# Optimization experiments

Hardware: AMD Instinct MI355X
Metric: run time of the kernel (lower is better)

The kernel has to match this reference:

```python
import jax, jax.numpy as jnp
import numpy as np

EPS = 1.1920929e-07  # float32 eps, matches torch.finfo(torch.float32).eps
QMAX = 127.0         # 2**(8-1)-1 for 8-bit symmetric quantization
NUM_HEADS = 12


def _round_ste(x):
    return x + jax.lax.stop_gradient(jnp.round(x) - x)


def _floor_ste(x):
    return x + jax.lax.stop_gradient(jnp.floor(x) - x)


def _act_quant(x):
    # per-tensor symmetric 8-bit (QuantAct + SymmetricQuantFunction)
    s = jax.lax.stop_gradient(jnp.maximum(jnp.max(jnp.abs(x)) / QMAX, EPS))
    return jnp.clip(_round_ste(x / s), -QMAX - 1.0, QMAX), s


def _weight_quant(w):
    # per-output-channel symmetric 8-bit (scale.view(-1,1) path in linear_quantize)
    s = jax.lax.stop_gradient(jnp.maximum(jnp.max(jnp.abs(w), axis=1) / QMAX, EPS))
    return jnp.clip(_round_ste(w / s[:, None]), -QMAX - 1.0, QMAX), s


def _fixedpoint_requant(pre_act, pre_s, z_s):
    # fixedpoint_mul: requantize int accumulator (value pre_act on scale pre_s)
    # onto scale z_s using a 31-bit mantissa/exponent decomposition (batch_frexp).
    def int_path(pa):
        z_int = jnp.round(pa / pre_s)
        ns = pre_s / z_s
        e = jnp.floor(jnp.log2(ns)) + 1.0          # frexp exponent: ns = m * 2**e, m in [0.5,1)
        m = jnp.floor(ns * jnp.exp2(-e) * 2.0 ** 31 + 0.5)  # ROUND_HALF_UP mantissa * 2**31
        out = jnp.round(z_int * m * jnp.exp2(e - 31.0))
        return jnp.clip(out, -QMAX - 1.0, QMAX)
    hard = jax.lax.stop_gradient(int_path(pre_act))
    soft = pre_act / z_s                            # STE backward: grad / z_scaling_factor
    return soft + jax.lax.stop_gradient(hard - soft)


def _int_softmax(x_int, sf, output_bit=8, n=15):
    # IntSoftmax (shiftmax) with int_exp_shift; x_int = logits / sf (integer-valued)
    x_int = x_int - jnp.max(x_int, axis=-1, keepdims=True)
    x_int = x_int + _floor_ste(x_int / 2.0) - _floor_ste(x_int / 16.0)
    x0 = jax.lax.stop_gradient(jnp.floor(-1.0 / sf))
    x_int = jnp.maximum(x_int, n * x0)
    q = _floor_ste(x_int / x0)
    r = x_int - x0 * q
    exp_int = jnp.clip(_floor_ste((r / 2.0 - x0) * jnp.exp2(n - q)), 0.0, None)
    esum = jnp.minimum(jnp.sum(exp_int, axis=-1, keepdims=True), 2.0 ** 31 - 1.0)
    factor = _floor_ste((2.0 ** 31 - 1.0) / esum)
    exp_int = _floor_ste(exp_int * factor / 2.0 ** (31 - output_bit + 1))
    return exp_int, 1.0 / 2.0 ** (output_bit - 1)


def setup_inputs() -> dict:
    key = jax.random.key(0)
    k1, k2, k3, k4, k5 = jax.random.split(key, 5)
    B, N, C = 8, 577, 768
    return {
        "x": jax.random.normal(k1, (B, N, C), dtype=jnp.float32),
        "w_qkv": jax.random.normal(k2, (3 * C, C), dtype=jnp.float32) * 0.02,
        "b_qkv": jax.random.normal(k3, (3 * C,), dtype=jnp.float32) * 0.01,
        "w_proj": jax.random.normal(k4, (C, C), dtype=jnp.float32) * 0.02,
        "b_proj": jax.random.normal(k5, (C,), dtype=jnp.float32) * 0.01,
    }


def reference(x, w_qkv, b_qkv, w_proj, b_proj):
    B, N, C = x.shape
    H = NUM_HEADS
    D = C // H
    # ---- quantize input activation and qkv weight, integer GEMM ----
    x_int, s_x = _act_quant(x)                         # [B,N,C] int-valued, scalar scale
    wq_int, s_wq = _weight_quant(w_qkv)                # [3C,C], per-channel scale [3C]
    acc_s = s_x * s_wq                                 # accumulator scale [3C]
    qkv_int = jnp.einsum('bnc,oc->bno', x_int, wq_int) + _round_ste(b_qkv / acc_s)
    qkv_f = qkv_int * acc_s                            # dequantized qkv [B,N,3C]
    # ---- requantize qkv to per-tensor 8-bit via fixed-point mul ----
    s_qkv = jax.lax.stop_gradient(jnp.maximum(jnp.max(jnp.abs(qkv_f)) / QMAX, EPS))
    qkv8 = _fixedpoint_requant(qkv_f, acc_s, s_qkv)    # int8-valued [B,N,3C]
    qkv8 = qkv8.reshape(B, N, 3, H, D).transpose(2, 0, 3, 1, 4)
    q, k, v = qkv8[0], qkv8[1], qkv8[2]                # each [B,H,N,D]
    # ---- integer attention logits; float scale carries head_dim**-0.5 ----
    attn_int = jnp.einsum('bhnd,bhmd->bhnm', q, k)
    s_attn = s_qkv * s_qkv * (D ** -0.5)
    sm_int, s_sm = _int_softmax(attn_int, s_attn)      # int probs on scale 1/128
    # ---- integer attn @ v ----
    ctx_int = jnp.einsum('bhnm,bhmd->bhnd', sm_int, v)
    ctx_f = (ctx_int * (s_sm * s_qkv)).transpose(0, 2, 1, 3).reshape(B, N, C)
    s_ctx = jax.lax.stop_gradient(jnp.maximum(jnp.max(jnp.abs(ctx_f)) / QMAX, EPS))
    ctx8 = _fixedpoint_requant(ctx_f, s_sm * s_qkv, s_ctx)
    # ---- quantized output projection ----
    wp_int, s_wp = _weight_quant(w_proj)
    out_s = s_ctx * s_wp
    out_int = jnp.einsum('bnc,oc->bno', ctx8, wp_int) + _round_ste(b_proj / out_s)
    return out_int * out_s
```

## Files before the change

### kernel.cpp

```cpp
#include <hip/hip_runtime.h>
#include <math.h>

#define BQ 8
#define SEQ 577
#define CH 768
#define NH 12
#define HD 64
#define M_ROWS (BQ * SEQ)
#define QKV_CH (3 * CH)
#define NX (M_ROWS * CH)
#define EPSF 1.1920929e-07f
#define F2P31 2147483648.0f

#define VT_ROW 640
#define P_STRIDE 688

#define NSLOT 64
#define SLOT_STRIDE 16

typedef __attribute__((ext_vector_type(4))) int i32x4;

__device__ __forceinline__ float slot_scale(const unsigned* __restrict__ s) {
  float m = 0.f;
#pragma unroll
  for (int i = 0; i < NSLOT; ++i) m = fmaxf(m, __uint_as_float(s[i * SLOT_STRIDE]));
  return fmaxf(m / 127.0f, EPSF);
}

__device__ __forceinline__ void mfma_gemm_core_lds(
    const signed char* __restrict__ A, const signed char* __restrict__ Bm,
    signed char* As, signed char* Bs,
    int arow0, int bcol0, int w, int lane, i32x4 acc[4][4]) {
  int c = lane & 15, q = lane >> 4;
  int lr = lane >> 2;
  int ksb = (lane & 3) << 4;
  const signed char* Aw = As + ((w & 1) << 12);
  const signed char* Bw = Bs + ((w >> 1) << 12);
  for (int k0 = 0; k0 < CH; k0 += 64) {
#pragma unroll
    for (int u = 0; u < 2; ++u) {
      int row = (w << 5) + (u << 4) + lr;
      __builtin_amdgcn_global_load_lds(
          (const __attribute__((address_space(1))) void*)(A + (size_t)(arow0 + row) * CH + k0 + ksb),
          (__attribute__((address_space(3))) void*)(As + (w << 11) + (u << 10)),
          16, 0, 0);
      __builtin_amdgcn_global_load_lds(
          (const __attribute__((address_space(1))) void*)(Bm + (size_t)(bcol0 + row) * CH + k0 + ksb),
          (__attribute__((address_space(3))) void*)(Bs + (w << 11) + (u << 10)),
          16, 0, 0);
    }
    __syncthreads();
    i32x4 af[4], bf[4];
#pragma unroll
    for (int i = 0; i < 4; ++i)
      af[i] = *(const i32x4*)(Aw + (((i << 4) + c) << 6) + (q << 4));
#pragma unroll
    for (int j = 0; j < 4; ++j)
      bf[j] = *(const i32x4*)(Bw + (((j << 4) + c) << 6) + (q << 4));
#pragma unroll
    for (int i = 0; i < 4; ++i)
#pragma unroll
      for (int j = 0; j < 4; ++j)
        acc[i][j] = __builtin_amdgcn_mfma_i32_16x16x64_i8(af[i], bf[j], acc[i][j], 0, 0, 0);
    __syncthreads();
  }
}

__global__ __launch_bounds__(256) void k_prep(
    const float* __restrict__ x, const float* __restrict__ w_qkv,
    const float* __restrict__ w_proj,
    signed char* __restrict__ WQ8, float* __restrict__ SWQ,
    signed char* __restrict__ WP8, float* __restrict__ SWP,
    unsigned* __restrict__ mxx) {
  __shared__ float red[4];
  int blk = blockIdx.x, tid = threadIdx.x;
  if (blk < QKV_CH + CH) {
    const float* wr; signed char* w8; float* sw; int r;
    if (blk < QKV_CH) { r = blk; wr = w_qkv + (size_t)r * CH; w8 = WQ8 + (size_t)r * CH; sw = SWQ; }
    else { r = blk - QKV_CH; wr = w_proj + (size_t)r * CH; w8 = WP8 + (size_t)r * CH; sw = SWP; }
    const float4* wr4 = (const float4*)wr;
    float4 v = {0.f, 0.f, 0.f, 0.f};
    float m = 0.f;
    if (tid < CH / 4) {
      v = wr4[tid];
      m = fmaxf(fmaxf(fabsf(v.x), fabsf(v.y)), fmaxf(fabsf(v.z), fabsf(v.w)));
    }
#pragma unroll
    for (int o = 32; o; o >>= 1) m = fmaxf(m, __shfl_xor(m, o, 64));
    if ((tid & 63) == 0) red[tid >> 6] = m;
    __syncthreads();
    float mm = fmaxf(fmaxf(red[0], red[1]), fmaxf(red[2], red[3]));
    float s = fmaxf(mm / 127.0f, EPSF);
    if (tid == 0) sw[r] = s;
    if (tid < CH / 4) {
      int pk = 0;
#pragma unroll
      for (int u = 0; u < 4; ++u) {
        float xv = (u == 0) ? v.x : (u == 1) ? v.y : (u == 2) ? v.z : v.w;
        float q = rintf(xv / s);
        q = fminf(fmaxf(q, -128.f), 127.f);
        pk |= ((int)(signed char)q & 0xff) << (u * 8);
      }
      ((int*)w8)[tid] = pk;
    }
  } else {
    int ab = blk - (QKV_CH + CH);
    const float4* x4 = (const float4*)x;
    float m = 0.f;
    for (int i = ab * 256 + tid; i < NX / 4; i += 1024 * 256) {
      float4 v = x4[i];
      m = fmaxf(m, fmaxf(fmaxf(fabsf(v.x), fabsf(v.y)), fmaxf(fabsf(v.z), fabsf(v.w))));
    }
#pragma unroll
    for (int o = 32; o; o >>= 1) m = fmaxf(m, __shfl_xor(m, o, 64));
    if ((tid & 63) == 0) red[tid >> 6] = m;
    __syncthreads();
    if (tid == 0)
      atomicMax(&mxx[(ab & (NSLOT - 1)) * SLOT_STRIDE],
                __float_as_uint(fmaxf(fmaxf(red[0], red[1]), fmaxf(red[2], red[3]))));
  }
}

__global__ void k_aquant(const float* __restrict__ x, int n,
                         const unsigned* __restrict__ mxx, signed char* __restrict__ x8) {
  float s = slot_scale(mxx);
  int n4 = n >> 2;
  const float4* x4 = (const float4*)x;
  int* dst = (int*)x8;
  int stride = gridDim.x * blockDim.x;
  for (int i = blockIdx.x * blockDim.x + threadIdx.x; i < n4; i += stride) {
    float4 v = x4[i];
    int pk = 0;
#pragma unroll
    for (int u = 0; u < 4; ++u) {
      float xv = (u == 0) ? v.x : (u == 1) ? v.y : (u == 2) ? v.z : v.w;
      float q = rintf(xv / s);
      q = fminf(fmaxf(q, -128.f), 127.f);
      pk |= ((int)(signed char)q & 0xff) << (u * 8);
    }
    dst[i] = pk;
  }
}

__global__ __launch_bounds__(256) void k_gemm_qkv(
    const signed char* __restrict__ A, const signed char* __restrict__ Bm,
    const float* __restrict__ swq, const float* __restrict__ bias,
    const unsigned* __restrict__ mxx, int* __restrict__ Cq, unsigned* __restrict__ mxq) {
  __shared__ __align__(16) signed char As[8192], Bs[8192];
  __shared__ float red[4];
  int t = threadIdx.x;
  int lane = t & 63, w = t >> 6;
  int c = lane & 15, q = lane >> 4;
  int arow = blockIdx.y * 128 + (w & 1) * 64;
  int bcol = blockIdx.x * 128 + (w >> 1) * 64;
  i32x4 acc[4][4] = {};
  mfma_gemm_core_lds(A, Bm, As, Bs, blockIdx.y * 128, blockIdx.x * 128, w, lane, acc);
  float s_x = slot_scale(mxx);
  float lmax = 0.f;
#pragma unroll
  for (int j = 0; j < 4; ++j) {
    int ccol = bcol + j * 16 + c;
    float accs = s_x * swq[ccol];
    int bint = (int)rintf(bias[ccol] / accs);
#pragma unroll
    for (int i = 0; i < 4; ++i)
#pragma unroll
      for (int r = 0; r < 4; ++r) {
        int rr = arow + i * 16 + q * 4 + r;
        if (rr < M_ROWS) {
          int qv = acc[i][j][r] + bint;
          Cq[(size_t)rr * QKV_CH + ccol] = qv;
          lmax = fmaxf(lmax, fabsf((float)qv * accs));
        }
      }
  }
#pragma unroll
  for (int off = 32; off; off >>= 1) lmax = fmaxf(lmax, __shfl_xor(lmax, off, 64));
  if (lane == 0) red[w] = lmax;
  __syncthreads();
  if (t == 0)
    atomicMax(&mxq[((blockIdx.y * 18 + blockIdx.x) & (NSLOT - 1)) * SLOT_STRIDE],
              __float_as_uint(fmaxf(fmaxf(red[0], red[1]), fmaxf(red[2], red[3]))));
}

#define QK_BLKS 870
__global__ __launch_bounds__(256) void k_qkv_requant(
    const int* __restrict__ Cq, const float* __restrict__ swq,
    const unsigned* __restrict__ mxx, const unsigned* __restrict__ mxq,
    signed char* __restrict__ Q8, signed char* __restrict__ K8,
    signed char* __restrict__ VT8) {
  float s_x = slot_scale(mxx);
  float s_qkv = slot_scale(mxq);
  int blk = blockIdx.x, tid = threadIdx.x;
  if (blk < QK_BLKS) {
    int bx = blk % 6, by = blk / 6;
    int o = bx * 256 + tid;
    float accs = s_x * swq[o];
    float ns = accs / s_qkv;
    int e; float f = frexpf(ns, &e);
    float mm = floorf(f * F2P31 + 0.5f);
    float pw = __int_as_float((e + 96) << 23);
    int isK = (o >= CH);
    int rem = o - (isK ? CH : 0);
    int h = rem >> 6, d = rem & 63;
    signed char* dstb = isK ? K8 : Q8;
    int bn0 = by * 32;
    int bnend = min(bn0 + 32, M_ROWS);
    for (int bn = bn0; bn < bnend; ++bn) {
      int qv = Cq[(size_t)bn * QKV_CH + o];
      float qf = (float)qv * accs;
      float z = rintf(qf / accs);
      float t8 = rintf((z * mm) * pw);
      t8 = fminf(fmaxf(t8, -128.f), 127.f);
      int b = bn / SEQ, n = bn - b * SEQ;
      dstb[(((size_t)(b * NH + h) * SEQ + n) << 6) + d] = (signed char)t8;
    }
  } else {
    __shared__ __align__(16) signed char VTt[64 * 68];
    int vt = blk - QK_BLKS;
    int bh = vt / 10, n0 = (vt - bh * 10) * 64;
    int b = bh / NH, h = bh - b * NH;
    int od = tid & 63;
    int o = 2 * CH + h * 64 + od;
    float accs = s_x * swq[o];
    float ns = accs / s_qkv;
    int e; float f = frexpf(ns, &e);
    float mm = floorf(f * F2P31 + 0.5f);
    float pw = __int_as_float((e + 96) << 23);
    int nr = tid >> 6;
    for (int p = 0; p < 16; ++p) {
      int nl = nr * 16 + p;
      int n = n0 + nl;
      signed char v = 0;
      if (n < SEQ) {
        int qv = Cq[(size_t)(b * SEQ + n) * QKV_CH + o];
        float qf = (float)qv * accs;
        float z = rintf(qf / accs);
        float t8 = rintf((z * mm) * pw);
        t8 = fminf(fmaxf(t8, -128.f), 127.f);
        v = (signed char)t8;
      }
      VTt[od * 68 + nl] = v;
    }
    __syncthreads();
    int w16 = tid & 15, dr = tid >> 4;
#pragma unroll
    for (int pp = 0; pp < 4; ++pp) {
      int d = pp * 16 + dr;
      int val = *(const int*)&VTt[d * 68 + w16 * 4];
      *(int*)(VT8 + (size_t)bh * (64 * VT_ROW) + (size_t)d * VT_ROW + n0 + w16 * 4) = val;
    }
  }
}

__global__ __launch_bounds__(256, 4) void k_attn(
    const signed char* __restrict__ Q8, const signed char* __restrict__ K8,
    const signed char* __restrict__ VT8, const unsigned* __restrict__ mxq,
    int* __restrict__ ctxi, unsigned* __restrict__ mxc) {
  __shared__ __align__(16) unsigned char P[16 * P_STRIDE];
  __shared__ int Rmax[4][16];
  __shared__ unsigned long long Rsum[4][16];
  __shared__ float Rav[4];
  int tid = threadIdx.x;
  int t = tid & 63, wid = tid >> 6;
  int lin = blockIdx.x;
  int j = lin >> 3;
  int bh = (lin & 7) * 12 + j / 37;
  int qt = j % 37;
  int b = bh / NH, h = bh - b * NH;
  int col = t & 15, q4 = t >> 4;
  const signed char* Qb = Q8 + (((size_t)bh * SEQ + qt * 16 + col) << 6);
  i32x4 qa = *(const i32x4*)(Qb + q4 * 16);
  const signed char* Kb = K8 + ((size_t)bh * SEQ << 6);
  int kt0 = wid * 10;
  i32x4 sv[10];
  bool vld[10];
  int mx[4] = {-2147483647 - 1, -2147483647 - 1, -2147483647 - 1, -2147483647 - 1};
#pragma unroll
  for (int u = 0; u < 10; ++u) {
    int kt = kt0 + u;
    int krow = min(kt * 16 + col, SEQ - 1);
    const signed char* kr = Kb + ((size_t)krow << 6);
    i32x4 kb = *(const i32x4*)(kr + q4 * 16);
    i32x4 a = {0, 0, 0, 0};
    a = __builtin_amdgcn_mfma_i32_16x16x64_i8(qa, kb, a, 0, 0, 0);
    sv[u] = a;
    bool valid = (kt < 36) | ((kt == 36) & (col < 1));
    vld[u] = valid;
#pragma unroll
    for (int r = 0; r < 4; ++r)
      if (valid) mx[r] = max(mx[r], a[r]);
  }
#pragma unroll
  for (int r = 0; r < 4; ++r) {
    mx[r] = max(mx[r], __shfl_xor(mx[r], 1, 64));
    mx[r] = max(mx[r], __shfl_xor(mx[r], 2, 64));
    mx[r] = max(mx[r], __shfl_xor(mx[r], 4, 64));
    mx[r] = max(mx[r], __shfl_xor(mx[r], 8, 64));
  }
  if (col == 0) {
#pragma unroll
    for (int r = 0; r < 4; ++r) Rmax[wid][q4 * 4 + r] = mx[r];
  }
  __syncthreads();
#pragma unroll
  for (int r = 0; r < 4; ++r) {
    int row = q4 * 4 + r;
    mx[r] = max(max(Rmax[0][row], Rmax[1][row]), max(Rmax[2][row], Rmax[3][row]));
  }
  float s_qkv = slot_scale(mxq);
  float s_attn = (s_qkv * s_qkv) * 0.125f;
  float x0f = floorf(-1.0f / s_attn);
  int x0i = (int)x0f;
  int bi = -x0i;
  int nx0i = 15 * x0i;
  int twob = bi << 1;
  unsigned Mq = 0xFFFFFFFFu / (unsigned)bi + 1u;
  bool bOne = (Mq == 0u);
  unsigned long long su[4] = {0ull, 0ull, 0ull, 0ull};
#pragma unroll
  for (int u = 0; u < 10; ++u) {
#pragma unroll
    for (int r = 0; r < 4; ++r) {
      int d = sv[u][r] - mx[r];
      int xi = d + (d >> 1) - (d >> 4);
      xi = max(xi, nx0i);
      xi = min(xi, 0);
      unsigned a = (unsigned)(-xi);
      unsigned q = bOne ? a : __umulhi(a, Mq);
      int rr = (int)(a - q * (unsigned)bi);
      unsigned m = (unsigned)(twob - rr);
      unsigned ue = (m << 15) >> (q + 1);
      ue = vld[u] ? ue : 0u;
      su[r] += ue;
      sv[u][r] = (int)ue;
    }
  }
#pragma unroll
  for (int r = 0; r < 4; ++r) {
    su[r] += __shfl_xor(su[r], 1, 64);
    su[r] += __shfl_xor(su[r], 2, 64);
    su[r] += __shfl_xor(su[r], 4, 64);
    su[r] += __shfl_xor(su[r], 8, 64);
  }
  if (col == 0) {
#pragma unroll
    for (int r = 0; r < 4; ++r) Rsum[wid][q4 * 4 + r] = su[r];
  }
  __syncthreads();
  float fac[4];
#pragma unroll
  for (int r = 0; r < 4; ++r) {
    int row = q4 * 4 + r;
    unsigned long long dv = ((Rsum[0][row] + Rsum[1][row]) + Rsum[2][row]) + Rsum[3][row];
    float esum = fminf((float)dv, F2P31);
    fac[r] = floorf(F2P31 / esum);
  }
#pragma unroll
  for (int u = 0; u < 10; ++u) {
    int kt = kt0 + u;
#pragma unroll
    for (int r = 0; r < 4; ++r) {
      float e = (float)(unsigned)sv[u][r];
      int p = (int)floorf((e * fac[r]) * 5.9604644775390625e-08f);
      P[(q4 * 4 + r) * P_STRIDE + kt * 16 + col] = (unsigned char)p;
    }
  }
  __syncthreads();
  const signed char* Vb = VT8 + (size_t)bh * (64 * VT_ROW);
  i32x4 ac0 = {0, 0, 0, 0}, ac1 = {0, 0, 0, 0};
#pragma unroll
  for (int mc = 0; mc < 10; mc += 2) {
    i32x4 pa0 = *(const i32x4*)&P[col * P_STRIDE + mc * 64 + q4 * 16];
    i32x4 vb0 = *(const i32x4*)(Vb + (size_t)(wid * 16 + col) * VT_ROW + mc * 64 + q4 * 16);
    ac0 = __builtin_amdgcn_mfma_i32_16x16x64_i8(pa0, vb0, ac0, 0, 0, 0);
    i32x4 pa1 = *(const i32x4*)&P[col * P_STRIDE + (mc + 1) * 64 + q4 * 16];
    i32x4 vb1 = *(const i32x4*)(Vb + (size_t)(wid * 16 + col) * VT_ROW + (mc + 1) * 64 + q4 * 16);
    ac1 = __builtin_amdgcn_mfma_i32_16x16x64_i8(pa1, vb1, ac1, 0, 0, 0);
  }
  float pre_s = 0.0078125f * s_qkv;
  float avmax = 0.f;
#pragma unroll
  for (int r = 0; r < 4; ++r) {
    int n = qt * 16 + q4 * 4 + r;
    if (n < SEQ) {
      int cacc = ac0[r] + ac1[r];
      ctxi[((size_t)(b * SEQ + n)) * CH + h * 64 + wid * 16 + col] = cacc;
      avmax = fmaxf(avmax, fabsf((float)cacc * pre_s));
    }
  }
#pragma unroll
  for (int off = 32; off; off >>= 1) avmax = fmaxf(avmax, __shfl_xor(avmax, off, 64));
  if (t == 0) Rav[wid] = avmax;
  __syncthreads();
  if (tid == 0)
    atomicMax(&mxc[(blockIdx.x & (NSLOT - 1)) * SLOT_STRIDE],
              __float_as_uint(fmaxf(fmaxf(Rav[0], Rav[1]), fmaxf(Rav[2], Rav[3]))));
}

__global__ void k_ctx_requant(const int* __restrict__ ctxi, const unsigned* __restrict__ mxq,
                              const unsigned* __restrict__ mxc, signed char* __restrict__ C8) {
  float s_qkv = slot_scale(mxq);
  float pre_s = 0.0078125f * s_qkv;
  float s_ctx = slot_scale(mxc);
  float ns = pre_s / s_ctx;
  int e;
  float f = frexpf(ns, &e);
  float mm = floorf(f * F2P31 + 0.5f);
  float pw = exp2f((float)e - 31.0f);
  int total4 = (M_ROWS * CH) / 4;
  int stride = gridDim.x * blockDim.x;
  const int4* src = (const int4*)ctxi;
  int* dst = (int*)C8;
  for (int i = blockIdx.x * blockDim.x + threadIdx.x; i < total4; i += stride) {
    int4 v = src[i];
    int pk = 0;
#pragma unroll
    for (int u = 0; u < 4; ++u) {
      int cv = (u == 0) ? v.x : (u == 1) ? v.y : (u == 2) ? v.z : v.w;
      float cf = (float)cv * pre_s;
      float z = rintf(cf / pre_s);
      float t8 = rintf((z * mm) * pw);
      t8 = fminf(fmaxf(t8, -128.f), 127.f);
      pk |= ((int)(signed char)t8 & 0xff) << (u * 8);
    }
    dst[i] = pk;
  }
}

__global__ __launch_bounds__(256) void k_gemm_out(
    const signed char* __restrict__ A, const signed char* __restrict__ Bm,
    const float* __restrict__ swp, const float* __restrict__ bias,
    const unsigned* __restrict__ mxc, float* __restrict__ outp) {
  __shared__ __align__(16) signed char As[8192], Bs[8192];
  int t = threadIdx.x;
  int lane = t & 63, w = t >> 6;
  int c = lane & 15, q = lane >> 4;
  int arow = blockIdx.y * 128 + (w & 1) * 64;
  int bcol = blockIdx.x * 128 + (w >> 1) * 64;
  i32x4 acc[4][4] = {};
  mfma_gemm_core_lds(A, Bm, As, Bs, blockIdx.y * 128, blockIdx.x * 128, w, lane, acc);
  float s_ctx = slot_scale(mxc);
#pragma unroll
  for (int j = 0; j < 4; ++j) {
    int ccol = bcol + j * 16 + c;
    float outs = s_ctx * swp[ccol];
    int bint = (int)rintf(bias[ccol] / outs);
#pragma unroll
    for (int i = 0; i < 4; ++i)
#pragma unroll
      for (int r = 0; r < 4; ++r) {
        int rr = arow + i * 16 + q * 4 + r;
        if (rr < M_ROWS)
          outp[(size_t)rr * CH + ccol] = (float)(acc[i][j][r] + bint) * outs;
      }
  }
}

extern "C" void kernel_launch(void* const* d_in, const int* in_sizes, int n_in,
                              void* d_out, int out_size, void* d_ws, size_t ws_size,
                              hipStream_t stream) {
  const float* x = (const float*)d_in[0];
  const float* w_qkv = (const float*)d_in[1];
  const float* b_qkv = (const float*)d_in[2];
  const float* w_proj = (const float*)d_in[3];
  const float* b_proj = (const float*)d_in[4];
  float* outp = (float*)d_out;

  char* ws = (char*)d_ws;
  size_t off = 0;
  auto alloc = [&](size_t sz) -> char* {
    char* p = ws + off;
    off = (off + sz + 4095) & ~(size_t)4095;
    return p;
  };
  unsigned* mxx = (unsigned*)alloc(3 * NSLOT * SLOT_STRIDE * 4);
  unsigned* mxq = mxx + NSLOT * SLOT_STRIDE;
  unsigned* mxc = mxq + NSLOT * SLOT_STRIDE;
  float* SWQ = (float*)alloc(QKV_CH * 4);
  float* SWP = (float*)alloc(CH * 4);
  signed char* WQ8 = (signed char*)alloc((size_t)QKV_CH * CH);
  signed char* WP8 = (signed char*)alloc((size_t)CH * CH);
  signed char* X8  = (signed char*)alloc((size_t)(M_ROWS + 128) * CH);
  signed char* Q8  = (signed char*)alloc((size_t)M_ROWS * CH);
  signed char* K8  = (signed char*)alloc((size_t)M_ROWS * CH);
  signed char* VT8 = (signed char*)alloc((size_t)BQ * NH * 64 * VT_ROW);
  signed char* C8  = (signed char*)alloc((size_t)(M_ROWS + 128) * CH);
  int* QKVI = (int*)alloc((size_t)M_ROWS * QKV_CH * 4);
  int* CTXI = (int*)alloc((size_t)M_ROWS * CH * 4);
  (void)ws_size;

  hipMemsetAsync(mxx, 0, 3 * NSLOT * SLOT_STRIDE * 4, stream);
  k_prep<<<QKV_CH + CH + 1024, 256, 0, stream>>>(x, w_qkv, w_proj, WQ8, SWQ, WP8, SWP, mxx);
  k_aquant<<<2048, 256, 0, stream>>>(x, NX, mxx, X8);
  dim3 g1(QKV_CH / 128, (M_ROWS + 127) / 128);
  k_gemm_qkv<<<g1, 256, 0, stream>>>(X8, WQ8, SWQ, b_qkv, mxx, QKVI, mxq);
  k_qkv_requant<<<QK_BLKS + BQ * NH * 10, 256, 0, stream>>>(QKVI, SWQ, mxx, mxq, Q8, K8, VT8);
  k_attn<<<37 * BQ * NH, 256, 0, stream>>>(Q8, K8, VT8, mxq, CTXI, mxc);
  k_ctx_requant<<<1024, 256, 0, stream>>>(CTXI, mxq, mxc, C8);
  dim3 g2(CH / 128, (M_ROWS + 127) / 128);
  k_gemm_out<<<g2, 256, 0, stream>>>(C8, WP8, SWP, b_proj, mxc, outp);
}
```

Measured before the change: 198.9 us.

## Use single-wave 64x64 GEMM tiles and a global exp lookup table in attention

Both int8 GEMMs now run as one-wave blocks on 64x64 tiles instead of four-wave 128x128 tiles, which gives many more blocks but less operand reuse per block. Separately, the requant kernel gets extra blocks that build a global table of shift-exp values indexed by the clamped logit, and the attention softmax reads that table instead of computing a divide and shift per element. The table lookup trades arithmetic for scattered global/L2 reads, and the table is capped in size, which may not cover large scale ratios.

```diff
diff --git a/kernel.cpp b/kernel.cpp
--- a/kernel.cpp
+++ b/kernel.cpp
@@ -14,6 +14,7 @@
 
 #define VT_ROW 640
 #define P_STRIDE 688
+#define TBL_CAP 245761
 
 #define NSLOT 64
 #define SLOT_STRIDE 16
@@ -27,36 +28,34 @@
   return fmaxf(m / 127.0f, EPSF);
 }
 
-__device__ __forceinline__ void mfma_gemm_core_lds(
+__device__ __forceinline__ void mfma_gemm_core_w1(
     const signed char* __restrict__ A, const signed char* __restrict__ Bm,
     signed char* As, signed char* Bs,
-    int arow0, int bcol0, int w, int lane, i32x4 acc[4][4]) {
+    int arow0, int bcol0, int lane, i32x4 acc[4][4]) {
   int c = lane & 15, q = lane >> 4;
   int lr = lane >> 2;
   int ksb = (lane & 3) << 4;
-  const signed char* Aw = As + ((w & 1) << 12);
-  const signed char* Bw = Bs + ((w >> 1) << 12);
   for (int k0 = 0; k0 < CH; k0 += 64) {
 #pragma unroll
-    for (int u = 0; u < 2; ++u) {
-      int row = (w << 5) + (u << 4) + lr;
+    for (int u = 0; u < 4; ++u) {
+      int row = (u << 4) + lr;
       __builtin_amdgcn_global_load_lds(
           (const __attribute__((address_space(1))) void*)(A + (size_t)(arow0 + row) * CH + k0 + ksb),
-          (__attribute__((address_space(3))) void*)(As + (w << 11) + (u << 10)),
+          (__attribute__((address_space(3))) void*)(As + (u << 10)),
           16, 0, 0);
       __builtin_amdgcn_global_load_lds(
           (const __attribute__((address_space(1))) void*)(Bm + (size_t)(bcol0 + row) * CH + k0 + ksb),
-          (__attribute__((address_space(3))) void*)(Bs + (w << 11) + (u << 10)),
+          (__attribute__((address_space(3))) void*)(Bs + (u << 10)),
           16, 0, 0);
     }
     __syncthreads();
     i32x4 af[4], bf[4];
 #pragma unroll
     for (int i = 0; i < 4; ++i)
-      af[i] = *(const i32x4*)(Aw + (((i << 4) + c) << 6) + (q << 4));
+      af[i] = *(const i32x4*)(As + (((i << 4) + c) << 6) + (q << 4));
 #pragma unroll
     for (int j = 0; j < 4; ++j)
-      bf[j] = *(const i32x4*)(Bw + (((j << 4) + c) << 6) + (q << 4));
+      bf[j] = *(const i32x4*)(Bs + (((j << 4) + c) << 6) + (q << 4));
 #pragma unroll
     for (int i = 0; i < 4; ++i)
 #pragma unroll
@@ -142,19 +141,17 @@
   }
 }
 
-__global__ __launch_bounds__(256) void k_gemm_qkv(
+__global__ __launch_bounds__(64) void k_gemm_qkv(
     const signed char* __restrict__ A, const signed char* __restrict__ Bm,
     const float* __restrict__ swq, const float* __restrict__ bias,
     const unsigned* __restrict__ mxx, int* __restrict__ Cq, unsigned* __restrict__ mxq) {
-  __shared__ __align__(16) signed char As[8192], Bs[8192];
-  __shared__ float red[4];
-  int t = threadIdx.x;
-  int lane = t & 63, w = t >> 6;
+  __shared__ __align__(16) signed char As[4096], Bs[4096];
+  int lane = threadIdx.x;
   int c = lane & 15, q = lane >> 4;
-  int arow = blockIdx.y * 128 + (w & 1) * 64;
-  int bcol = blockIdx.x * 128 + (w >> 1) * 64;
+  int arow = blockIdx.y * 64;
+  int bcol = blockIdx.x * 64;
   i32x4 acc[4][4] = {};
-  mfma_gemm_core_lds(A, Bm, As, Bs, blockIdx.y * 128, blockIdx.x * 128, w, lane, acc);
+  mfma_gemm_core_w1(A, Bm, As, Bs, arow, bcol, lane, acc);
   float s_x = slot_scale(mxx);
   float lmax = 0.f;
 #pragma unroll
@@ -176,19 +173,18 @@
   }
 #pragma unroll
   for (int off = 32; off; off >>= 1) lmax = fmaxf(lmax, __shfl_xor(lmax, off, 64));
-  if (lane == 0) red[w] = lmax;
-  __syncthreads();
-  if (t == 0)
-    atomicMax(&mxq[((blockIdx.y * 18 + blockIdx.x) & (NSLOT - 1)) * SLOT_STRIDE],
-              __float_as_uint(fmaxf(fmaxf(red[0], red[1]), fmaxf(red[2], red[3]))));
+  if (lane == 0)
+    atomicMax(&mxq[((blockIdx.y * 36 + blockIdx.x) & (NSLOT - 1)) * SLOT_STRIDE],
+              __float_as_uint(lmax));
 }
 
 #define QK_BLKS 870
+#define V_BLKS (BQ * NH * 10)
 __global__ __launch_bounds__(256) void k_qkv_requant(
     const int* __restrict__ Cq, const float* __restrict__ swq,
     const unsigned* __restrict__ mxx, const unsigned* __restrict__ mxq,
     signed char* __restrict__ Q8, signed char* __restrict__ K8,
-    signed char* __restrict__ VT8) {
+    signed char* __restrict__ VT8, unsigned* __restrict__ TexpG) {
   float s_x = slot_scale(mxx);
   float s_qkv = slot_scale(mxq);
   int blk = blockIdx.x, tid = threadIdx.x;
@@ -215,7 +211,7 @@
       int b = bn / SEQ, n = bn - b * SEQ;
       dstb[(((size_t)(b * NH + h) * SEQ + n) << 6) + d] = (signed char)t8;
     }
-  } else {
+  } else if (blk < QK_BLKS + V_BLKS) {
     __shared__ __align__(16) signed char VTt[64 * 68];
     int vt = blk - QK_BLKS;
     int bh = vt / 10, n0 = (vt - bh * 10) * 64;
@@ -250,12 +246,26 @@
       int val = *(const int*)&VTt[d * 68 + w16 * 4];
       *(int*)(VT8 + (size_t)bh * (64 * VT_ROW) + (size_t)d * VT_ROW + n0 + w16 * 4) = val;
     }
+  } else {
+    int tb = blk - (QK_BLKS + V_BLKS);
+    float s_attn = (s_qkv * s_qkv) * 0.125f;
+    int bi = -(int)floorf(-1.0f / s_attn);
+    int tblN = min(15 * bi + 1, TBL_CAP);
+    unsigned Mq = 0xFFFFFFFFu / (unsigned)bi + 1u;
+    bool bOne = (Mq == 0u);
+    int twob = bi << 1;
+    for (int a = tb * 256 + tid; a < tblN; a += 4 * 256) {
+      unsigned q = bOne ? (unsigned)a : __umulhi((unsigned)a, Mq);
+      unsigned rr = (unsigned)a - q * (unsigned)bi;
+      TexpG[a] = ((unsigned)(twob - (int)rr) << 14) >> q;
+    }
   }
 }
 
 __global__ __launch_bounds__(256, 4) void k_attn(
     const signed char* __restrict__ Q8, const signed char* __restrict__ K8,
     const signed char* __restrict__ VT8, const unsigned* __restrict__ mxq,
+    const unsigned* __restrict__ TexpG,
     int* __restrict__ ctxi, unsigned* __restrict__ mxc) {
   __shared__ __align__(16) unsigned char P[16 * P_STRIDE];
   __shared__ int Rmax[4][16];
@@ -312,11 +322,7 @@
   float s_attn = (s_qkv * s_qkv) * 0.125f;
   float x0f = floorf(-1.0f / s_attn);
   int x0i = (int)x0f;
-  int bi = -x0i;
   int nx0i = 15 * x0i;
-  int twob = bi << 1;
-  unsigned Mq = 0xFFFFFFFFu / (unsigned)bi + 1u;
-  bool bOne = (Mq == 0u);
   unsigned long long su[4] = {0ull, 0ull, 0ull, 0ull};
 #pragma unroll
   for (int u = 0; u < 10; ++u) {
@@ -326,11 +332,7 @@
       int xi = d + (d >> 1) - (d >> 4);
       xi = max(xi, nx0i);
       xi = min(xi, 0);
-      unsigned a = (unsigned)(-xi);
-      unsigned q = bOne ? a : __umulhi(a, Mq);
-      int rr = (int)(a - q * (unsigned)bi);
-      unsigned m = (unsigned)(twob - rr);
-      unsigned ue = (m << 15) >> (q + 1);
+      unsigned ue = TexpG[-xi];
       ue = vld[u] ? ue : 0u;
       su[r] += ue;
       sv[u][r] = (int)ue;
@@ -428,18 +430,17 @@
   }
 }
 
-__global__ __launch_bounds__(256) void k_gemm_out(
+__global__ __launch_bounds__(64) void k_gemm_out(
     const signed char* __restrict__ A, const signed char* __restrict__ Bm,
     const float* __restrict__ swp, const float* __restrict__ bias,
     const unsigned* __restrict__ mxc, float* __restrict__ outp) {
-  __shared__ __align__(16) signed char As[8192], Bs[8192];
-  int t = threadIdx.x;
-  int lane = t & 63, w = t >> 6;
+  __shared__ __align__(16) signed char As[4096], Bs[4096];
+  int lane = threadIdx.x;
   int c = lane & 15, q = lane >> 4;
-  int arow = blockIdx.y * 128 + (w & 1) * 64;
-  int bcol = blockIdx.x * 128 + (w >> 1) * 64;
+  int arow = blockIdx.y * 64;
+  int bcol = blockIdx.x * 64;
   i32x4 acc[4][4] = {};
-  mfma_gemm_core_lds(A, Bm, As, Bs, blockIdx.y * 128, blockIdx.x * 128, w, lane, acc);
+  mfma_gemm_core_w1(A, Bm, As, Bs, arow, bcol, lane, acc);
   float s_ctx = slot_scale(mxc);
 #pragma unroll
   for (int j = 0; j < 4; ++j) {
@@ -477,6 +478,7 @@
   unsigned* mxx = (unsigned*)alloc(3 * NSLOT * SLOT_STRIDE * 4);
   unsigned* mxq = mxx + NSLOT * SLOT_STRIDE;
   unsigned* mxc = mxq + NSLOT * SLOT_STRIDE;
+  unsigned* TexpG = (unsigned*)alloc((size_t)TBL_CAP * 4);
   float* SWQ = (float*)alloc(QKV_CH * 4);
   float* SWP = (float*)alloc(CH * 4);
   signed char* WQ8 = (signed char*)alloc((size_t)QKV_CH * CH);
@@ -493,11 +495,11 @@
   hipMemsetAsync(mxx, 0, 3 * NSLOT * SLOT_STRIDE * 4, stream);
   k_prep<<<QKV_CH + CH + 1024, 256, 0, stream>>>(x, w_qkv, w_proj, WQ8, SWQ, WP8, SWP, mxx);
   k_aquant<<<2048, 256, 0, stream>>>(x, NX, mxx, X8);
-  dim3 g1(QKV_CH / 128, (M_ROWS + 127) / 128);
-  k_gemm_qkv<<<g1, 256, 0, stream>>>(X8, WQ8, SWQ, b_qkv, mxx, QKVI, mxq);
-  k_qkv_requant<<<QK_BLKS + BQ * NH * 10, 256, 0, stream>>>(QKVI, SWQ, mxx, mxq, Q8, K8, VT8);
-  k_attn<<<37 * BQ * NH, 256, 0, stream>>>(Q8, K8, VT8, mxq, CTXI, mxc);
+  dim3 g1(QKV_CH / 64, (M_ROWS + 63) / 64);
+  k_gemm_qkv<<<g1, 64, 0, stream>>>(X8, WQ8, SWQ, b_qkv, mxx, QKVI, mxq);
+  k_qkv_requant<<<QK_BLKS + V_BLKS + 4, 256, 0, stream>>>(QKVI, SWQ, mxx, mxq, Q8, K8, VT8, TexpG);
+  k_attn<<<37 * BQ * NH, 256, 0, stream>>>(Q8, K8, VT8, mxq, TexpG, CTXI, mxc);
   k_ctx_requant<<<1024, 256, 0, stream>>>(CTXI, mxq, mxc, C8);
-  dim3 g2(CH / 128, (M_ROWS + 127) / 128);
-  k_gemm_out<<<g2, 256, 0, stream>>>(C8, WP8, SWP, b_proj, mxc, outp);
-}
+  dim3 g2(CH / 64, (M_ROWS + 63) / 64);
+  k_gemm_out<<<g2, 64, 0, stream>>>(C8, WP8, SWP, b_proj, mxc, outp);
+}
```

Result: slower. 278.8 us (+40.2%).
